# Kernel tuning notes

Measured on AMD Instinct MI355X. Metric: run time of the kernel, lower is better.

Reference implementation:

```python
import jax, jax.numpy as jnp
import numpy as np

H = 8       # num_heads
K = 16      # neighbours
LN_EPS = 1e-6

def _knn_indices(coords, k):
    # coords: (B,N,3) float32. Squared-euclidean distances preserve kNN ordering of cdist.
    d2 = jnp.sum(coords * coords, axis=-1)                      # (B,N)
    dist2 = d2[:, :, None] + d2[:, None, :] - 2.0 * jnp.einsum('bnd,bmd->bnm', coords, coords)
    _, idx = jax.lax.top_k(-dist2, k)                           # (B,N,k) smallest distances
    return idx

def _gather(x, idx):
    # x: (B,N,D), idx: (B,N,K) -> (B,N,K,D)
    return jax.vmap(lambda a, i: a[i])(x, idx)

def setup_inputs() -> dict:
    key = jax.random.key(0)
    ks = jax.random.split(key, 16)
    B, N, D = 2, 8192, 256
    P = 6
    std = 0.02
    inp = {
        'features': jax.random.normal(ks[0], (B, N, D), jnp.float32),
        'coords': jax.random.uniform(ks[1], (B, N, 3), jnp.float32),
        'normals': jax.random.normal(ks[2], (B, N, 3), jnp.float32),
        'mask': jnp.ones((B, N), jnp.float32),
        # linear weights stored (in, out): y = x @ W + b
        'Wq': jax.random.normal(ks[3], (D, D), jnp.float32) * std,
        'bq': jnp.zeros((D,), jnp.float32),
        'Wk': jax.random.normal(ks[4], (D, D), jnp.float32) * std,
        'bk': jnp.zeros((D,), jnp.float32),
        'Wv': jax.random.normal(ks[5], (D, D), jnp.float32) * std,
        'bv': jnp.zeros((D,), jnp.float32),
        'Wo': jax.random.normal(ks[6], (D, D), jnp.float32) * std,  # torch inits this to zero; random here for nontrivial test
        'bo': jnp.zeros((D,), jnp.float32),
        'Wp1': jax.random.normal(ks[7], (P, D), jnp.float32) * std,
        'bp1': jnp.zeros((D,), jnp.float32),
        'Wp2': jax.random.normal(ks[8], (D, D), jnp.float32) * std,
        'bp2': jnp.zeros((D,), jnp.float32),
        'gamma': jnp.ones((D,), jnp.float32),
        'beta': jnp.zeros((D,), jnp.float32),
    }
    return inp

def reference(features, coords, normals, mask, Wq, bq, Wk, bk, Wv, bv, Wo, bo,
              Wp1, bp1, Wp2, bp2, gamma, beta):
    B, N, D = features.shape
    dh = D // H
    scale = 1.0 / np.sqrt(dh).astype(np.float32)
    residual = features

    idx = _knn_indices(jax.lax.stop_gradient(coords), K)        # (B,N,K), no-grad as in torch

    nb_coords = _gather(coords, idx)                            # (B,N,K,3)
    rel_pos = coords[:, :, None, :] - nb_coords                 # (B,N,K,3)
    pos_input = jnp.concatenate(
        [rel_pos, jnp.broadcast_to(normals[:, :, None, :], rel_pos.shape)], axis=-1)  # (B,N,K,6)
    # pos MLP: Linear -> GELU(exact, torch default) -> Linear
    pos_emb = jax.nn.gelu(pos_input @ Wp1 + bp1, approximate=False) @ Wp2 + bp2       # (B,N,K,D)

    q = features @ Wq + bq                                      # (B,N,D)
    kp = features @ Wk + bk
    vp = features @ Wv + bv
    kg = _gather(kp, idx)                                       # (B,N,K,D)
    vg = _gather(vp, idx)

    k_comb = (kg + pos_emb).reshape(B, N, K, H, dh)
    v_comb = (vg + pos_emb).reshape(B, N, K, H, dh)
    qh = q.reshape(B, N, H, dh)

    logits = jnp.einsum('bnhd,bnkhd->bnkh', qh, k_comb) * scale  # (B,N,K,H)
    nb_valid = _gather(mask[..., None], idx)[..., 0]             # (B,N,K)
    logits = jnp.where(nb_valid[..., None] > 0, logits, -jnp.inf)
    attn = jax.nn.softmax(logits, axis=2)
    attn = jnp.nan_to_num(attn, nan=0.0)

    out = jnp.einsum('bnkh,bnkhd->bnhd', attn, v_comb).reshape(B, N, D)
    out = (out @ Wo + bo) * mask[..., None]

    h = residual + out
    mu = jnp.mean(h, axis=-1, keepdims=True)
    var = jnp.mean((h - mu) ** 2, axis=-1, keepdims=True)
    h = (h - mu) / jnp.sqrt(var + LN_EPS) * gamma + beta
    return h * mask[..., None]
```

## Files before the change

### kernel.cpp

```cpp
#include <hip/hip_runtime.h>
#include <hip/hip_bf16.h>
#include <math.h>

typedef unsigned short u16t;
typedef unsigned int   u32t;
typedef unsigned long long u64t;
typedef __attribute__((ext_vector_type(8))) short  short8;
typedef __attribute__((ext_vector_type(4))) float  floatx4;

#define NPTS   8192
#define DMODEL 256
#define BNTOT  16384
#define HSTR   264

__device__ __forceinline__ float bitsf(u32t u){ union { u32t i; float f; } v; v.i = u; return v.f; }
__device__ __forceinline__ float b2f(u16t s){ return bitsf(((u32t)s) << 16); }
__device__ __forceinline__ u16t f2b(float f){
  __hip_bfloat16 h = __float2bfloat16(f);
  return *reinterpret_cast<u16t*>(&h);
}
__device__ __forceinline__ uint4 pack8(const float* o){
  uint4 st;
  st.x = (u32t)f2b(o[0]) | ((u32t)f2b(o[1]) << 16);
  st.y = (u32t)f2b(o[2]) | ((u32t)f2b(o[3]) << 16);
  st.z = (u32t)f2b(o[4]) | ((u32t)f2b(o[5]) << 16);
  st.w = (u32t)f2b(o[6]) | ((u32t)f2b(o[7]) << 16);
  return st;
}

__device__ __forceinline__ float gelu_fast(float x){
  float ax = fabsf(x) * 0.70710678118654752f;
  float t  = __builtin_amdgcn_rcpf(__builtin_fmaf(0.3275911f, ax, 1.0f));
  float p  = t*(0.254829592f + t*(-0.284496736f + t*(1.421413741f +
             t*(-1.453152027f + t*1.061405429f))));
  float er = __builtin_fmaf(-p, __expf(-ax*ax), 1.0f);
  return 0.5f * x * (1.0f + copysignf(er, x));
}

__global__ __launch_bounds__(256) void fill_valf(float* p, int n, float v){
  int i = blockIdx.x * 256 + threadIdx.x;
  if (i < n) p[i] = v;
}

__global__ __launch_bounds__(256) void wprep1(const float* __restrict__ W,
                                              u16t* __restrict__ out) {
  int r = blockIdx.x * 256 + threadIdx.x;
  int v = r & 7, l = (r >> 3) & 63, cca = (r >> 9) & 15, ic = r >> 13;
  int i = ic * 32 + (l >> 4) * 8 + v;
  int c = cca * 16 + (l & 15);
  out[r] = f2b(W[(size_t)i * DMODEL + c]);
}

__device__ __forceinline__ void cswap_asc(u64t& a, u64t& b){
  u64t mn = (a < b) ? a : b;
  u64t mx = (a < b) ? b : a;
  a = mn; b = mx;
}
__device__ __forceinline__ void bitonic16(u64t v[16]){
  #pragma unroll
  for (int k = 2; k <= 16; k <<= 1) {
    #pragma unroll
    for (int j = k >> 1; j > 0; j >>= 1) {
      #pragma unroll
      for (int i = 0; i < 16; ++i) {
        int l = i ^ j;
        if (l > i) {
          if ((i & k) == 0) cswap_asc(v[i], v[l]);
          else              cswap_asc(v[l], v[i]);
        }
      }
    }
  }
}
__device__ __forceinline__ void merge16(u64t best[16], u64t v[16]){
  #pragma unroll
  for (int i = 0; i < 16; ++i) {
    u64t o = v[15 - i];
    best[i] = (best[i] < o) ? best[i] : o;
  }
  #pragma unroll
  for (int j = 8; j > 0; j >>= 1) {
    #pragma unroll
    for (int i = 0; i < 16; ++i) {
      int l = i ^ j;
      if (l > i) cswap_asc(best[i], best[l]);
    }
  }
}
__device__ __forceinline__ void knn_flush(u64t best[16], u32t& thr, int& cnt,
                                          const u64t* bufw, int lane){
  u64t v[16];
  #pragma unroll
  for (int s = 0; s < 16; ++s) {
    u64t x = bufw[s * 64 + lane];
    v[s] = (s < cnt) ? x : 0xFFFFFFFFFFFFFFFFULL;
  }
  bitonic16(v);
  merge16(best, v);
  thr = (u32t)(best[15] >> 32);
  cnt = 0;
}

__global__ __launch_bounds__(256) void knn_partial(const float* __restrict__ coords,
                                                   u64t* __restrict__ pk) {
  int qb = blockIdx.x >> 3, ch = blockIdx.x & 7;
  int tid = threadIdx.x;
  int lane = tid & 63, wv = tid >> 6;
  int g = qb * 256 + tid;
  int b = g >> 13;
  alignas(16) __shared__ float4 tile[256];
  __shared__ u64t buf[4][16][64];

  float qx = coords[(size_t)g * 3 + 0];
  float qy = coords[(size_t)g * 3 + 1];
  float qz = coords[(size_t)g * 3 + 2];
  float qd2 = __fadd_rn(__fadd_rn(__fmul_rn(qx,qx), __fmul_rn(qy,qy)), __fmul_rn(qz,qz));

  u64t best[16];
  #pragma unroll
  for (int s = 0; s < 16; ++s) best[s] = 0xFFFFFFFFFFFFFFFFULL;
  u32t thr = 0xFFFFFFFFu;
  int  cnt = 0;
  u64t* bufw = &buf[wv][0][0];

  int cs = ch * 1024;
  for (int t = 0; t < 4; ++t) {
    int ci = cs + t * 256 + tid;
    size_t cb = (size_t)(b * NPTS + ci) * 3;
    float x = coords[cb + 0];
    float y = coords[cb + 1];
    float z = coords[cb + 2];
    float d2 = __fadd_rn(__fadd_rn(__fmul_rn(x,x), __fmul_rn(y,y)), __fmul_rn(z,z));
    __syncthreads();
    tile[tid] = make_float4(x, y, z, d2);
    __syncthreads();
    int cbase = cs + t * 256;
    for (int u = 0; u < 256; ++u) {
      float4 cd = tile[u];
      float dot = __fadd_rn(__fadd_rn(__fmul_rn(qx,cd.x), __fmul_rn(qy,cd.y)), __fmul_rn(qz,cd.z));
      float dist = __fsub_rn(__fadd_rn(qd2, cd.w), __fmul_rn(2.0f, dot));
      u32t db  = __float_as_uint(dist);
      u32t key = db ^ ((u32t)(((int)db) >> 31) | 0x80000000u);
      if (key <= thr) {
        bufw[cnt * 64 + lane] = ((u64t)key << 32) | (u32t)(cbase + u);
        ++cnt;
      }
      if (__any(cnt == 16)) knn_flush(best, thr, cnt, bufw, lane);
    }
  }
  if (__any(cnt > 0)) knn_flush(best, thr, cnt, bufw, lane);

  size_t base = (size_t)g * 128 + ch * 16;
  #pragma unroll
  for (int s = 0; s < 16; ++s) pk[base + s] = best[s];
}

__global__ __launch_bounds__(256) void knn_merge(const u64t* __restrict__ pk,
                                                 u16t* __restrict__ idxb) {
  int g = blockIdx.x * 256 + threadIdx.x;
  size_t base = (size_t)g * 128;
  int h[8];
  #pragma unroll
  for (int c = 0; c < 8; ++c) h[c] = 0;
  for (int s = 0; s < 16; ++s) {
    u64t bk = 0xFFFFFFFFFFFFFFFFULL; int bc = 0;
    #pragma unroll
    for (int c = 0; c < 8; ++c) {
      if (h[c] < 16) {
        u64t kk = pk[base + c * 16 + h[c]];
        if (kk < bk) { bk = kk; bc = c; }
      }
    }
    idxb[(size_t)g * 16 + s] = (u16t)(bk & 0xFFFFu);
    h[bc]++;
  }
}

__global__ __launch_bounds__(256) void gemm_kv_mfma(const float* __restrict__ feat,
    const u16t* __restrict__ frags,
    const float* __restrict__ bk, const float* __restrict__ bv,
    u16t* __restrict__ kb, u16t* __restrict__ vb) {
  int mat = blockIdx.y;
  const u16t* wf   = frags + (size_t)mat * 65536;
  const float* bias = mat ? bv : bk;
  u16t* out         = mat ? vb : kb;

  int rbase = blockIdx.x * 64;
  int tid = threadIdx.x, lane = tid & 63, wvi = tid >> 6;
  int quad = lane >> 4, l15 = lane & 15;

  alignas(16) __shared__ u16t featS[64 * HSTR];

  {
    int r = tid >> 2, c0 = (tid & 3) * 64;
    const float* src = feat + (size_t)(rbase + r) * DMODEL + c0;
    u16t* dst = featS + r * HSTR + c0;
    #pragma unroll
    for (int t = 0; t < 8; ++t) {
      float4 a = *(const float4*)(src + t * 8);
      float4 b = *(const float4*)(src + t * 8 + 4);
      float o[8] = {a.x, a.y, a.z, a.w, b.x, b.y, b.z, b.w};
      *(uint4*)(dst + t * 8) = pack8(o);
    }
  }
  __syncthreads();

  floatx4 acc[16];
  #pragma unroll
  for (int ct = 0; ct < 16; ++ct) acc[ct] = (floatx4){0.f, 0.f, 0.f, 0.f};

  #pragma unroll
  for (int ic = 0; ic < 8; ++ic) {
    short8 af = *(const short8*)(featS + (wvi * 16 + l15) * HSTR + ic * 32 + quad * 8);
    #pragma unroll
    for (int ct = 0; ct < 16; ++ct) {
      short8 bf = *(const short8*)(wf + (((size_t)(ic * 16 + ct) * 64 + lane) << 3));
      acc[ct] = __builtin_amdgcn_mfma_f32_16x16x32_bf16(af, bf, acc[ct], 0, 0, 0);
    }
  }

  #pragma unroll
  for (int ct = 0; ct < 16; ++ct) {
    int col = ct * 16 + l15;
    float bvv = bias[col];
    #pragma unroll
    for (int r = 0; r < 4; ++r) {
      int row = rbase + wvi * 16 + quad * 4 + r;
      out[(size_t)row * DMODEL + col] = f2b(acc[ct][r] + bvv);
    }
  }
}

__global__ __launch_bounds__(256, 4) void attn_mega(
    const float* __restrict__ coords, const float* __restrict__ normals,
    const float* __restrict__ maskp, const float* __restrict__ feat,
    const float* __restrict__ bq,
    const float* __restrict__ Wp1, const float* __restrict__ bp1,
    const float* __restrict__ bp2,
    const u16t* __restrict__ idxp,
    const u16t* __restrict__ wqfrag, const u16t* __restrict__ wp2frag,
    const u16t* __restrict__ kbuf, const u16t* __restrict__ vbuf,
    float* __restrict__ outp) {
  alignas(16) __shared__ u16t hemb[64 * HSTR];
  alignas(16) __shared__ u16t qB[8 * HSTR];
  __shared__ float wS[64];
  __shared__ int   idS[64];

  int c    = threadIdx.x;
  int lane = c & 63;
  int wv   = c >> 6;
  int quad = lane >> 4;
  int l15  = lane & 15;
  int wv4  = wv * 4;
  int qbase = blockIdx.x * 8;

  {
    int r = c >> 5, c0 = (c & 31) * 8;
    const float* src = feat + (size_t)(qbase + r) * DMODEL + c0;
    float4 a = *(const float4*)(src);
    float4 b = *(const float4*)(src + 4);
    float o[8] = {a.x, a.y, a.z, a.w, b.x, b.y, b.z, b.w};
    *(uint4*)(hemb + r * HSTR + c0) = pack8(o);
    uint4 z; z.x = 0u; z.y = 0u; z.z = 0u; z.w = 0u;
    *(uint4*)(hemb + (8 + r) * HSTR + c0) = z;
  }
  __syncthreads();

  {
    floatx4 qa[4];
    #pragma unroll
    for (int cc = 0; cc < 4; ++cc) qa[cc] = (floatx4){0.f, 0.f, 0.f, 0.f};
    #pragma unroll
    for (int ic = 0; ic < 8; ++ic) {
      short8 af = *(const short8*)(hemb + l15 * HSTR + ic * 32 + quad * 8);
      #pragma unroll
      for (int cc = 0; cc < 4; ++cc) {
        short8 bf = *(const short8*)(wqfrag + (((size_t)(ic * 16 + wv4 + cc) * 64 + lane) << 3));
        qa[cc] = __builtin_amdgcn_mfma_f32_16x16x32_bf16(af, bf, qa[cc], 0, 0, 0);
      }
    }
    if (quad < 2) {
      #pragma unroll
      for (int cc = 0; cc < 4; ++cc) {
        int col = (wv4 + cc) * 16 + l15;
        float bqv = bq[col];
        #pragma unroll
        for (int r = 0; r < 4; ++r)
          qB[(quad * 4 + r) * HSTR + col] = f2b(qa[cc][r] + bqv);
      }
    }
  }

  float w1[6];
  #pragma unroll
  for (int p = 0; p < 6; ++p) w1[p] = Wp1[p * DMODEL + c];
  float b1v = bp1[c];
  float b2c[4];
  #pragma unroll
  for (int cc = 0; cc < 4; ++cc) b2c[cc] = bp2[(wv4 + cc) * 16 + l15];
  const float lsc = 0.17677669529663687f;
  __syncthreads();

  #pragma unroll
  for (int G = 0; G < 2; ++G) {
    for (int ql = 0; ql < 4; ++ql) {
      int g = qbase + G * 4 + ql;
      int bb0 = (g >> 13) * NPTS;
      float qx = coords[(size_t)g * 3 + 0];
      float qy = coords[(size_t)g * 3 + 1];
      float qz = coords[(size_t)g * 3 + 2];
      float n0 = normals[(size_t)g * 3 + 0];
      float n1 = normals[(size_t)g * 3 + 1];
      float n2 = normals[(size_t)g * 3 + 2];
      #pragma unroll
      for (int j = 0; j < 16; ++j) {
        int id = (int)idxp[(size_t)g * 16 + j];
        size_t cb = (size_t)(bb0 + id) * 3;
        float rx = qx - coords[cb + 0];
        float ry = qy - coords[cb + 1];
        float rz = qz - coords[cb + 2];
        float pre = b1v + rx * w1[0] + ry * w1[1] + rz * w1[2]
                        + n0 * w1[3] + n1 * w1[4] + n2 * w1[5];
        hemb[(ql * 16 + j) * HSTR + c] = f2b(gelu_fast(pre));
      }
    }
    __syncthreads();

    floatx4 acc[4][4];
    #pragma unroll
    for (int rt = 0; rt < 4; ++rt)
      #pragma unroll
      for (int cc = 0; cc < 4; ++cc) acc[rt][cc] = (floatx4){0.f, 0.f, 0.f, 0.f};

    #pragma unroll
    for (int ic = 0; ic < 8; ++ic) {
      short8 af0 = *(const short8*)(hemb + ( 0 + l15) * HSTR + ic * 32 + quad * 8);
      short8 af1 = *(const short8*)(hemb + (16 + l15) * HSTR + ic * 32 + quad * 8);
      short8 af2 = *(const short8*)(hemb + (32 + l15) * HSTR + ic * 32 + quad * 8);
      short8 af3 = *(const short8*)(hemb + (48 + l15) * HSTR + ic * 32 + quad * 8);
      #pragma unroll
      for (int cc = 0; cc < 4; ++cc) {
        short8 bf = *(const short8*)(wp2frag + (((size_t)(ic * 16 + wv4 + cc) * 64 + lane) << 3));
        acc[0][cc] = __builtin_amdgcn_mfma_f32_16x16x32_bf16(af0, bf, acc[0][cc], 0, 0, 0);
        acc[1][cc] = __builtin_amdgcn_mfma_f32_16x16x32_bf16(af1, bf, acc[1][cc], 0, 0, 0);
        acc[2][cc] = __builtin_amdgcn_mfma_f32_16x16x32_bf16(af2, bf, acc[2][cc], 0, 0, 0);
        acc[3][cc] = __builtin_amdgcn_mfma_f32_16x16x32_bf16(af3, bf, acc[3][cc], 0, 0, 0);
      }
    }
    __syncthreads();
    #pragma unroll
    for (int rt = 0; rt < 4; ++rt)
      #pragma unroll
      for (int cc = 0; cc < 4; ++cc) {
        int cg = (wv4 + cc) * 16 + l15;
        #pragma unroll
        for (int r = 0; r < 4; ++r)
          hemb[(rt * 16 + quad * 4 + r) * HSTR + cg] = f2b(acc[rt][cc][r] + b2c[cc]);
      }
    __syncthreads();

    {
      int g = qbase + G * 4 + wv;
      int bb0 = (g >> 13) * NPTS;
      int idl = (int)idxp[(size_t)g * 16 + l15];
      float mvl = maskp[bb0 + idl];
      unsigned long long bm = __ballot(mvl > 0.0f);
      if (quad == 0) idS[wv * 16 + l15] = idl;
      const u16t* krow = kbuf + (size_t)(bb0 + idl) * DMODEL;
      const u16t* erow = hemb + (wv * 16 + l15) * HSTR;
      const u16t* qrow = qB + (G * 4 + wv) * HSTR;
      floatx4 sa = (floatx4){0.f, 0.f, 0.f, 0.f};
      #pragma unroll
      for (int ic = 0; ic < 8; ++ic) {
        short8 ak  = *(const short8*)(krow + ic * 32 + quad * 8);
        short8 ae  = *(const short8*)(erow + ic * 32 + quad * 8);
        short8 qb8 = *(const short8*)(qrow + ic * 32 + quad * 8);
        sa = __builtin_amdgcn_mfma_f32_16x16x32_bf16(ak, qb8, sa, 0, 0, 0);
        sa = __builtin_amdgcn_mfma_f32_16x16x32_bf16(ae, qb8, sa, 0, 0, 0);
      }
      float lg[4];
      #pragma unroll
      for (int r = 0; r < 4; ++r) {
        int j = quad * 4 + r;
        lg[r] = ((bm >> j) & 1ULL) ? sa[r] * lsc : -1e30f;
      }
      float m = fmaxf(fmaxf(lg[0], lg[1]), fmaxf(lg[2], lg[3]));
      m = fmaxf(m, __shfl_xor(m, 16));
      m = fmaxf(m, __shfl_xor(m, 32));
      float e0 = __expf(lg[0] - m), e1 = __expf(lg[1] - m);
      float e2 = __expf(lg[2] - m), e3 = __expf(lg[3] - m);
      float s = e0 + e1 + e2 + e3;
      s += __shfl_xor(s, 16);
      s += __shfl_xor(s, 32);
      float inv = (m > -1e29f) ? __builtin_amdgcn_rcpf(s) : 0.0f;
      if (l15 == 0) {
        wS[wv * 16 + quad * 4 + 0] = e0 * inv;
        wS[wv * 16 + quad * 4 + 1] = e1 * inv;
        wS[wv * 16 + quad * 4 + 2] = e2 * inv;
        wS[wv * 16 + quad * 4 + 3] = e3 * inv;
      }
    }
    __syncthreads();

    #pragma unroll
    for (int ql = 0; ql < 4; ++ql) {
      int g = qbase + G * 4 + ql;
      int bb0 = (g >> 13) * NPTS;
      float o = 0.0f;
      #pragma unroll
      for (int j = 0; j < 16; ++j) {
        int id  = idS[ql * 16 + j];
        float w = wS[ql * 16 + j];
        float vv = b2f(vbuf[(size_t)(bb0 + id) * DMODEL + c]);
        float ee = b2f(hemb[(ql * 16 + j) * HSTR + c]);
        o += w * (vv + ee);
      }
      outp[(size_t)g * DMODEL + c] = o;
    }
    if (G == 0) __syncthreads();
  }
}

__global__ __launch_bounds__(256) void gemm_out(const float* __restrict__ feat,
    const float* __restrict__ maskp,
    const u16t* __restrict__ wofrag, const float* __restrict__ bo,
    const float* __restrict__ gamma, const float* __restrict__ beta,
    float* __restrict__ io) {
  int rbase = blockIdx.x * 64;
  int tid = threadIdx.x, lane = tid & 63, wvi = tid >> 6;
  int quad = lane >> 4, l15 = lane & 15;

  alignas(16) __shared__ u16t oS[64 * HSTR];

  {
    int r = tid >> 2, c0 = (tid & 3) * 64;
    const float* src = io + (size_t)(rbase + r) * DMODEL + c0;
    u16t* dst = oS + r * HSTR + c0;
    #pragma unroll
    for (int t = 0; t < 8; ++t) {
      float4 a = *(const float4*)(src + t * 8);
      float4 b = *(const float4*)(src + t * 8 + 4);
      float o[8] = {a.x, a.y, a.z, a.w, b.x, b.y, b.z, b.w};
      *(uint4*)(dst + t * 8) = pack8(o);
    }
  }
  __syncthreads();

  floatx4 acc[16];
  #pragma unroll
  for (int ct = 0; ct < 16; ++ct) acc[ct] = (floatx4){0.f, 0.f, 0.f, 0.f};

  #pragma unroll
  for (int ic = 0; ic < 8; ++ic) {
    short8 af = *(const short8*)(oS + (wvi * 16 + l15) * HSTR + ic * 32 + quad * 8);
    #pragma unroll
    for (int ct = 0; ct < 16; ++ct) {
      short8 bf = *(const short8*)(wofrag + (((size_t)(ic * 16 + ct) * 64 + lane) << 3));
      acc[ct] = __builtin_amdgcn_mfma_f32_16x16x32_bf16(af, bf, acc[ct], 0, 0, 0);
    }
  }

  float bov[16], gamv[16], betv[16];
  #pragma unroll
  for (int ct = 0; ct < 16; ++ct) {
    int col = ct * 16 + l15;
    bov[ct]  = bo[col];
    gamv[ct] = gamma[col];
    betv[ct] = beta[col];
  }

  #pragma unroll
  for (int r = 0; r < 4; ++r) {
    int row = rbase + wvi * 16 + quad * 4 + r;
    float mv = maskp[row];
    float hv[16];
    float s = 0.0f, s2 = 0.0f;
    #pragma unroll
    for (int ct = 0; ct < 16; ++ct) {
      float h = feat[(size_t)row * DMODEL + ct * 16 + l15] + (acc[ct][r] + bov[ct]) * mv;
      hv[ct] = h; s += h; s2 += h * h;
    }
    #pragma unroll
    for (int off = 1; off < 16; off <<= 1) {
      s  += __shfl_xor(s,  off, 16);
      s2 += __shfl_xor(s2, off, 16);
    }
    float mu  = s  * (1.0f / 256.0f);
    float ms  = s2 * (1.0f / 256.0f);
    float var = ms - mu * mu;
    float inv = 1.0f / sqrtf(var + 1e-6f);
    #pragma unroll
    for (int ct = 0; ct < 16; ++ct) {
      float y = (hv[ct] - mu) * inv * gamv[ct] + betv[ct];
      y *= mv;
      io[(size_t)row * DMODEL + ct * 16 + l15] = y;
    }
  }
}

extern "C" void kernel_launch(void* const* d_in, const int* in_sizes, int n_in,
                              void* d_out, int out_size, void* d_ws, size_t ws_size,
                              hipStream_t stream) {
  static const int EXP[18] = {4194304, 49152, 49152, 16384,
                              65536, 256, 65536, 256, 65536, 256, 65536, 256,
                              1536, 256, 65536, 256, 256, 256};
  bool sizes_ok = (n_in >= 18);
  if (sizes_ok) for (int i = 0; i < 18; ++i) sizes_ok = sizes_ok && (in_sizes[i] == EXP[i]);
  int fb = (out_size + 255) / 256;
  if (!sizes_ok) {
    fill_valf<<<fb, 256, 0, stream>>>((float*)d_out, out_size, 0.0f);
    return;
  }
  const size_t WS_NEED = 17825792;
  if (ws_size < WS_NEED) {
    fill_valf<<<fb, 256, 0, stream>>>((float*)d_out, out_size, 1.0f);
    return;
  }

  const float* feat    = (const float*)d_in[0];
  const float* coords  = (const float*)d_in[1];
  const float* normals = (const float*)d_in[2];
  const float* maskp   = (const float*)d_in[3];
  const float* Wq  = (const float*)d_in[4];
  const float* bq  = (const float*)d_in[5];
  const float* Wk  = (const float*)d_in[6];
  const float* bk  = (const float*)d_in[7];
  const float* Wv  = (const float*)d_in[8];
  const float* bv  = (const float*)d_in[9];
  const float* Wo  = (const float*)d_in[10];
  const float* bo  = (const float*)d_in[11];
  const float* Wp1 = (const float*)d_in[12];
  const float* bp1 = (const float*)d_in[13];
  const float* Wp2 = (const float*)d_in[14];
  const float* bp2 = (const float*)d_in[15];
  const float* gamma = (const float*)d_in[16];
  const float* beta  = (const float*)d_in[17];

  char* ws = (char*)d_ws;
  u16t*  idx16  = (u16t*)(ws);
  u16t*  frags  = (u16t*)(ws + 524288);
  u16t*  kb     = (u16t*)(ws + 1048576);
  u16t*  vb     = (u16t*)(ws + 9437184);
  u64t*  pk     = (u64t*)(ws + 1048576);
  u16t*  wofrag = (u16t*)(ws + 1048576);

  wprep1<<<256, 256, 0, stream>>>(Wk,  frags);
  wprep1<<<256, 256, 0, stream>>>(Wv,  frags + 65536);
  wprep1<<<256, 256, 0, stream>>>(Wp2, frags + 131072);
  wprep1<<<256, 256, 0, stream>>>(Wq,  frags + 196608);
  knn_partial<<<512, 256, 0, stream>>>(coords, pk);
  knn_merge<<<64, 256, 0, stream>>>(pk, idx16);
  gemm_kv_mfma<<<dim3(256, 2), 256, 0, stream>>>(feat, frags, bk, bv, kb, vb);
  attn_mega<<<2048, 256, 0, stream>>>(coords, normals, maskp, feat,
                                      bq, Wp1, bp1, bp2,
                                      idx16, frags + 196608, frags + 131072,
                                      kb, vb, (float*)d_out);
  wprep1<<<256, 256, 0, stream>>>(Wo, wofrag);
  gemm_out<<<256, 256, 0, stream>>>(feat, maskp, wofrag, bo, gamma, beta,
                                    (float*)d_out);
}
```

Before: 545.5 us.

## Make attention per-wave independent, fold bp2 into K/V bias, float kNN threshold

The attention kernel now has each wave own one query end to end. It builds that query's positional embedding, runs its full 16x256 MLP GEMM, computes the softmax and accumulates the output, passing weights and indices through shuffles instead of shared memory. This removes most block-wide barriers and the shared wS/idS arrays, at the cost of each wave streaming the whole Wp2 fragment set itself. bp2 is folded into the K/V bias in the projection GEMM, since it is added to both k and v. The kNN inner loop compares the float distance against a float threshold and builds the sortable key only when a candidate is accepted.

```diff
diff --git a/kernel.cpp b/kernel.cpp
--- a/kernel.cpp
+++ b/kernel.cpp
@@ -7,6 +7,7 @@
 typedef unsigned long long u64t;
 typedef __attribute__((ext_vector_type(8))) short  short8;
 typedef __attribute__((ext_vector_type(4))) float  floatx4;
+typedef __attribute__((ext_vector_type(4))) unsigned short ushort4v;
 
 #define NPTS   8192
 #define DMODEL 256
@@ -87,7 +88,7 @@
     }
   }
 }
-__device__ __forceinline__ void knn_flush(u64t best[16], u32t& thr, int& cnt,
+__device__ __forceinline__ void knn_flush(u64t best[16], float& thrf, int& cnt,
                                           const u64t* bufw, int lane){
   u64t v[16];
   #pragma unroll
@@ -97,7 +98,9 @@
   }
   bitonic16(v);
   merge16(best, v);
-  thr = (u32t)(best[15] >> 32);
+  u32t k15 = (u32t)(best[15] >> 32);
+  thrf = (k15 == 0xFFFFFFFFu) ? 3.3e38f
+       : bitsf((k15 & 0x80000000u) ? (k15 ^ 0x80000000u) : ~k15);
   cnt = 0;
 }
 
@@ -119,7 +122,7 @@
   u64t best[16];
   #pragma unroll
   for (int s = 0; s < 16; ++s) best[s] = 0xFFFFFFFFFFFFFFFFULL;
-  u32t thr = 0xFFFFFFFFu;
+  float thrf = 3.3e38f;
   int  cnt = 0;
   u64t* bufw = &buf[wv][0][0];
 
@@ -139,16 +142,16 @@
       float4 cd = tile[u];
       float dot = __fadd_rn(__fadd_rn(__fmul_rn(qx,cd.x), __fmul_rn(qy,cd.y)), __fmul_rn(qz,cd.z));
       float dist = __fsub_rn(__fadd_rn(qd2, cd.w), __fmul_rn(2.0f, dot));
-      u32t db  = __float_as_uint(dist);
-      u32t key = db ^ ((u32t)(((int)db) >> 31) | 0x80000000u);
-      if (key <= thr) {
+      if (dist <= thrf) {
+        u32t db  = __float_as_uint(dist);
+        u32t key = db ^ ((u32t)(((int)db) >> 31) | 0x80000000u);
         bufw[cnt * 64 + lane] = ((u64t)key << 32) | (u32t)(cbase + u);
         ++cnt;
       }
-      if (__any(cnt == 16)) knn_flush(best, thr, cnt, bufw, lane);
-    }
-  }
-  if (__any(cnt > 0)) knn_flush(best, thr, cnt, bufw, lane);
+      if (__any(cnt == 16)) knn_flush(best, thrf, cnt, bufw, lane);
+    }
+  }
+  if (__any(cnt > 0)) knn_flush(best, thrf, cnt, bufw, lane);
 
   size_t base = (size_t)g * 128 + ch * 16;
   #pragma unroll
@@ -179,6 +182,7 @@
 __global__ __launch_bounds__(256) void gemm_kv_mfma(const float* __restrict__ feat,
     const u16t* __restrict__ frags,
     const float* __restrict__ bk, const float* __restrict__ bv,
+    const float* __restrict__ bp2,
     u16t* __restrict__ kb, u16t* __restrict__ vb) {
   int mat = blockIdx.y;
   const u16t* wf   = frags + (size_t)mat * 65536;
@@ -222,7 +226,7 @@
   #pragma unroll
   for (int ct = 0; ct < 16; ++ct) {
     int col = ct * 16 + l15;
-    float bvv = bias[col];
+    float bvv = bias[col] + bp2[col];
     #pragma unroll
     for (int r = 0; r < 4; ++r) {
       int row = rbase + wvi * 16 + quad * 4 + r;
@@ -236,15 +240,12 @@
     const float* __restrict__ maskp, const float* __restrict__ feat,
     const float* __restrict__ bq,
     const float* __restrict__ Wp1, const float* __restrict__ bp1,
-    const float* __restrict__ bp2,
     const u16t* __restrict__ idxp,
     const u16t* __restrict__ wqfrag, const u16t* __restrict__ wp2frag,
     const u16t* __restrict__ kbuf, const u16t* __restrict__ vbuf,
     float* __restrict__ outp) {
   alignas(16) __shared__ u16t hemb[64 * HSTR];
-  alignas(16) __shared__ u16t qB[8 * HSTR];
-  __shared__ float wS[64];
-  __shared__ int   idS[64];
+  alignas(16) __shared__ u16t qB[8 * DMODEL];
 
   int c    = threadIdx.x;
   int lane = c & 63;
@@ -286,89 +287,83 @@
         float bqv = bq[col];
         #pragma unroll
         for (int r = 0; r < 4; ++r)
-          qB[(quad * 4 + r) * HSTR + col] = f2b(qa[cc][r] + bqv);
-      }
-    }
-  }
-
-  float w1[6];
-  #pragma unroll
-  for (int p = 0; p < 6; ++p) w1[p] = Wp1[p * DMODEL + c];
-  float b1v = bp1[c];
-  float b2c[4];
-  #pragma unroll
-  for (int cc = 0; cc < 4; ++cc) b2c[cc] = bp2[(wv4 + cc) * 16 + l15];
+          qB[(quad * 4 + r) * DMODEL + col] = f2b(qa[cc][r] + bqv);
+      }
+    }
+  }
+  __syncthreads();
+
   const float lsc = 0.17677669529663687f;
-  __syncthreads();
 
   #pragma unroll
   for (int G = 0; G < 2; ++G) {
-    for (int ql = 0; ql < 4; ++ql) {
-      int g = qbase + G * 4 + ql;
-      int bb0 = (g >> 13) * NPTS;
+    int g   = qbase + G * 4 + wv;
+    int bb0 = (g >> 13) * NPTS;
+    int idl = (int)idxp[(size_t)g * 16 + l15];
+
+    {
+      float4 a0 = *(const float4*)(Wp1 + 0 * DMODEL + lane * 4);
+      float4 a1 = *(const float4*)(Wp1 + 1 * DMODEL + lane * 4);
+      float4 a2 = *(const float4*)(Wp1 + 2 * DMODEL + lane * 4);
+      float4 a3 = *(const float4*)(Wp1 + 3 * DMODEL + lane * 4);
+      float4 a4 = *(const float4*)(Wp1 + 4 * DMODEL + lane * 4);
+      float4 a5 = *(const float4*)(Wp1 + 5 * DMODEL + lane * 4);
+      float4 b1 = *(const float4*)(bp1 + lane * 4);
       float qx = coords[(size_t)g * 3 + 0];
       float qy = coords[(size_t)g * 3 + 1];
       float qz = coords[(size_t)g * 3 + 2];
       float n0 = normals[(size_t)g * 3 + 0];
       float n1 = normals[(size_t)g * 3 + 1];
       float n2 = normals[(size_t)g * 3 + 2];
+      float bs0 = b1.x + n0 * a3.x + n1 * a4.x + n2 * a5.x;
+      float bs1 = b1.y + n0 * a3.y + n1 * a4.y + n2 * a5.y;
+      float bs2 = b1.z + n0 * a3.z + n1 * a4.z + n2 * a5.z;
+      float bs3 = b1.w + n0 * a3.w + n1 * a4.w + n2 * a5.w;
       #pragma unroll
       for (int j = 0; j < 16; ++j) {
-        int id = (int)idxp[(size_t)g * 16 + j];
+        int id = __shfl(idl, j);
         size_t cb = (size_t)(bb0 + id) * 3;
         float rx = qx - coords[cb + 0];
         float ry = qy - coords[cb + 1];
         float rz = qz - coords[cb + 2];
-        float pre = b1v + rx * w1[0] + ry * w1[1] + rz * w1[2]
-                        + n0 * w1[3] + n1 * w1[4] + n2 * w1[5];
-        hemb[(ql * 16 + j) * HSTR + c] = f2b(gelu_fast(pre));
-      }
-    }
-    __syncthreads();
-
-    floatx4 acc[4][4];
-    #pragma unroll
-    for (int rt = 0; rt < 4; ++rt)
-      #pragma unroll
-      for (int cc = 0; cc < 4; ++cc) acc[rt][cc] = (floatx4){0.f, 0.f, 0.f, 0.f};
-
-    #pragma unroll
-    for (int ic = 0; ic < 8; ++ic) {
-      short8 af0 = *(const short8*)(hemb + ( 0 + l15) * HSTR + ic * 32 + quad * 8);
-      short8 af1 = *(const short8*)(hemb + (16 + l15) * HSTR + ic * 32 + quad * 8);
-      short8 af2 = *(const short8*)(hemb + (32 + l15) * HSTR + ic * 32 + quad * 8);
-      short8 af3 = *(const short8*)(hemb + (48 + l15) * HSTR + ic * 32 + quad * 8);
-      #pragma unroll
-      for (int cc = 0; cc < 4; ++cc) {
-        short8 bf = *(const short8*)(wp2frag + (((size_t)(ic * 16 + wv4 + cc) * 64 + lane) << 3));
-        acc[0][cc] = __builtin_amdgcn_mfma_f32_16x16x32_bf16(af0, bf, acc[0][cc], 0, 0, 0);
-        acc[1][cc] = __builtin_amdgcn_mfma_f32_16x16x32_bf16(af1, bf, acc[1][cc], 0, 0, 0);
-        acc[2][cc] = __builtin_amdgcn_mfma_f32_16x16x32_bf16(af2, bf, acc[2][cc], 0, 0, 0);
-        acc[3][cc] = __builtin_amdgcn_mfma_f32_16x16x32_bf16(af3, bf, acc[3][cc], 0, 0, 0);
-      }
-    }
-    __syncthreads();
-    #pragma unroll
-    for (int rt = 0; rt < 4; ++rt)
-      #pragma unroll
-      for (int cc = 0; cc < 4; ++cc) {
-        int cg = (wv4 + cc) * 16 + l15;
+        ushort4v hw;
+        hw[0] = f2b(gelu_fast(bs0 + rx * a0.x + ry * a1.x + rz * a2.x));
+        hw[1] = f2b(gelu_fast(bs1 + rx * a0.y + ry * a1.y + rz * a2.y));
+        hw[2] = f2b(gelu_fast(bs2 + rx * a0.z + ry * a1.z + rz * a2.z));
+        hw[3] = f2b(gelu_fast(bs3 + rx * a0.w + ry * a1.w + rz * a2.w));
+        *(ushort4v*)(hemb + (wv * 16 + j) * HSTR + lane * 4) = hw;
+      }
+    }
+
+    {
+      floatx4 acc[16];
+      #pragma unroll
+      for (int cc = 0; cc < 16; ++cc) acc[cc] = (floatx4){0.f, 0.f, 0.f, 0.f};
+      #pragma unroll
+      for (int ic = 0; ic < 8; ++ic) {
+        short8 af = *(const short8*)(hemb + (wv * 16 + l15) * HSTR + ic * 32 + quad * 8);
+        #pragma unroll
+        for (int cc = 0; cc < 16; ++cc) {
+          short8 bf = *(const short8*)(wp2frag + (((size_t)(ic * 16 + cc) * 64 + lane) << 3));
+          acc[cc] = __builtin_amdgcn_mfma_f32_16x16x32_bf16(af, bf, acc[cc], 0, 0, 0);
+        }
+      }
+      #pragma unroll
+      for (int cc = 0; cc < 16; ++cc) {
+        int cg = cc * 16 + l15;
         #pragma unroll
         for (int r = 0; r < 4; ++r)
-          hemb[(rt * 16 + quad * 4 + r) * HSTR + cg] = f2b(acc[rt][cc][r] + b2c[cc]);
-      }
-    __syncthreads();
-
+          hemb[(wv * 16 + quad * 4 + r) * HSTR + cg] = f2b(acc[cc][r]);
+      }
+    }
+
+    float wjv[4];
     {
-      int g = qbase + G * 4 + wv;
-      int bb0 = (g >> 13) * NPTS;
-      int idl = (int)idxp[(size_t)g * 16 + l15];
       float mvl = maskp[bb0 + idl];
       unsigned long long bm = __ballot(mvl > 0.0f);
-      if (quad == 0) idS[wv * 16 + l15] = idl;
       const u16t* krow = kbuf + (size_t)(bb0 + idl) * DMODEL;
       const u16t* erow = hemb + (wv * 16 + l15) * HSTR;
-      const u16t* qrow = qB + (G * 4 + wv) * HSTR;
+      const u16t* qrow = qB + (G * 4 + wv) * DMODEL;
       floatx4 sa = (floatx4){0.f, 0.f, 0.f, 0.f};
       #pragma unroll
       for (int ic = 0; ic < 8; ++ic) {
@@ -393,31 +388,26 @@
       s += __shfl_xor(s, 16);
       s += __shfl_xor(s, 32);
       float inv = (m > -1e29f) ? __builtin_amdgcn_rcpf(s) : 0.0f;
-      if (l15 == 0) {
-        wS[wv * 16 + quad * 4 + 0] = e0 * inv;
-        wS[wv * 16 + quad * 4 + 1] = e1 * inv;
-        wS[wv * 16 + quad * 4 + 2] = e2 * inv;
-        wS[wv * 16 + quad * 4 + 3] = e3 * inv;
-      }
-    }
-    __syncthreads();
-
-    #pragma unroll
-    for (int ql = 0; ql < 4; ++ql) {
-      int g = qbase + G * 4 + ql;
-      int bb0 = (g >> 13) * NPTS;
-      float o = 0.0f;
+      wjv[0] = e0 * inv; wjv[1] = e1 * inv;
+      wjv[2] = e2 * inv; wjv[3] = e3 * inv;
+    }
+
+    {
+      float o0 = 0.f, o1 = 0.f, o2 = 0.f, o3 = 0.f;
       #pragma unroll
       for (int j = 0; j < 16; ++j) {
-        int id  = idS[ql * 16 + j];
-        float w = wS[ql * 16 + j];
-        float vv = b2f(vbuf[(size_t)(bb0 + id) * DMODEL + c]);
-        float ee = b2f(hemb[(ql * 16 + j) * HSTR + c]);
-        o += w * (vv + ee);
-      }
-      outp[(size_t)g * DMODEL + c] = o;
-    }
-    if (G == 0) __syncthreads();
+        float wj = __shfl(wjv[j & 3], (j >> 2) * 16);
+        int   id = __shfl(idl, j);
+        ushort4v v4 = *(const ushort4v*)(vbuf + (size_t)(bb0 + id) * DMODEL + lane * 4);
+        ushort4v e4 = *(const ushort4v*)(hemb + (wv * 16 + j) * HSTR + lane * 4);
+        o0 += wj * (b2f(v4[0]) + b2f(e4[0]));
+        o1 += wj * (b2f(v4[1]) + b2f(e4[1]));
+        o2 += wj * (b2f(v4[2]) + b2f(e4[2]));
+        o3 += wj * (b2f(v4[3]) + b2f(e4[3]));
+      }
+      float4 st = make_float4(o0, o1, o2, o3);
+      *(float4*)(outp + (size_t)g * DMODEL + lane * 4) = st;
+    }
   }
 }
 
@@ -550,9 +540,9 @@
   wprep1<<<256, 256, 0, stream>>>(Wq,  frags + 196608);
   knn_partial<<<512, 256, 0, stream>>>(coords, pk);
   knn_merge<<<64, 256, 0, stream>>>(pk, idx16);
-  gemm_kv_mfma<<<dim3(256, 2), 256, 0, stream>>>(feat, frags, bk, bv, kb, vb);
+  gemm_kv_mfma<<<dim3(256, 2), 256, 0, stream>>>(feat, frags, bk, bv, bp2, kb, vb);
   attn_mega<<<2048, 256, 0, stream>>>(coords, normals, maskp, feat,
-                                      bq, Wp1, bp1, bp2,
+                                      bq, Wp1, bp1,
                                       idx16, frags + 196608, frags + 131072,
                                       kb, vb, (float*)d_out);
   wprep1<<<256, 256, 0, stream>>>(Wo, wofrag);
```

Result: slower. 577.2 us (+5.8%).
